# Kernel optimization log

Hardware: AMD Instinct MI355X
Metric: run time of the kernel (lower is better)

## Reference

```python
import jax, jax.numpy as jnp
import numpy as np
from jax import lax

# module hyperparams (from init_kwargs)
IN_C, OUT_C, K, STRIDE, PAD, DIL = 256, 512, 3, 1, 1, 1
IN_SIZE = IN_C * K * K            # 2304
SIZE = 1 << int(np.ceil(np.log2(IN_SIZE)))  # 4096, in_size_extended
NSTACK = int(np.ceil(OUT_C / SIZE))          # 1
BATCH, H, W = 16, 32, 32


def fwht(x):
    """Unnormalized fast Walsh-Hadamard transform along last axis (n = power of 2).
    Matches torch.mm(hadamard(n), x.T).T / cyfht. O(n log n) butterfly."""
    n = x.shape[-1]
    orig_shape = x.shape
    x = x.reshape(-1, n)
    h = 1
    while h < n:
        x = x.reshape(-1, n // (2 * h), 2, h)
        a, b = x[:, :, 0, :], x[:, :, 1, :]
        x = jnp.stack([a + b, a - b], axis=2).reshape(-1, n)
        h *= 2
    return x.reshape(orig_shape)


def setup_inputs() -> dict:
    key = jax.random.key(0)
    k1, k2, k3, k4, k5, k6 = jax.random.split(key, 6)
    inp = jax.random.normal(k1, (BATCH, IN_C, H, W), dtype=jnp.float32)
    # B, G, S ~ N(0, 0.1) as in __init__
    B = 0.1 * jax.random.normal(k2, (NSTACK, SIZE), dtype=jnp.float32)
    G = 0.1 * jax.random.normal(k3, (NSTACK, SIZE), dtype=jnp.float32)
    S = 0.1 * jax.random.normal(k4, (NSTACK, SIZE), dtype=jnp.float32)
    bound = 1.0 / np.sqrt(IN_SIZE)
    bias = jax.random.uniform(k5, (OUT_C,), minval=-bound, maxval=bound, dtype=jnp.float32)
    P = jax.random.permutation(k6, NSTACK * SIZE)  # int32 permutation buffer
    return {"input": inp, "B": B, "G": G, "S": S, "bias": bias, "P": P}


def _pre_process(x):
    b, c, h, w = x.shape
    h_out = (h + 2 * PAD - DIL * (K - 1) - 1) // STRIDE + 1
    w_out = (h + 2 * PAD - DIL * (K - 1) - 1) // STRIDE + 1  # original uses h for w_out too
    # patches: (b, c*K*K, h_out, w_out), feature dim ordered (c, kh, kw) like F.unfold
    patches = lax.conv_general_dilated_patches(
        x, (K, K), (STRIDE, STRIDE), [(PAD, PAD), (PAD, PAD)],
        rhs_dilation=(DIL, DIL), dimension_numbers=("NCHW", "OIHW", "NCHW"))
    # view(b, c, K*K, L).permute(0,3,2,1).reshape(b*L, K*K*c)  -> kk-major, c-minor features
    L = h_out * w_out
    out = patches.reshape(b, c, K * K, L).transpose(0, 3, 2, 1).reshape(b * L, K * K * c)
    out = jnp.pad(out, ((0, 0), (0, SIZE - IN_SIZE)))
    return out, h_out, w_out


def reference(input, B, G, S, bias, P):
    b = input.shape[0]
    x, h_out, w_out = _pre_process(input)          # (b*L, SIZE)
    # diag B (nstack=1), FWHT, permutation, diag G, FWHT, diag S
    x = B.reshape(-1)[None, :] * x
    x = fwht(x)
    x = x[:, P]
    x = G.reshape(-1)[None, :] * x
    x = fwht(x)
    x = S.reshape(-1)[None, :] * x
    out = x[:, :OUT_C] + bias                      # (b*L, OUT_C)
    return out.reshape(b, h_out * w_out, OUT_C).transpose(0, 2, 1).reshape(b, OUT_C, h_out, w_out)
```

## Files before the change

### kernel.cpp

```cpp
#include <hip/hip_runtime.h>
#include <hip/hip_bf16.h>
#include <stdint.h>


typedef _Float16 h2 __attribute__((ext_vector_type(2)));

__device__ __forceinline__ uint16_t f2h16(float f) {
    union { _Float16 h; uint16_t u; } c; c.h = (_Float16)f; return c.u;
}
__device__ __forceinline__ int swz(int j) {
    return j ^ ((j >> 5) & 7) ^ (((j >> 8) & 1) * 24) ^ (((j >> 9) & 1) * 8);
}
__device__ __forceinline__ uint32_t h2u(h2 v) {
    union { h2 h; uint32_t u; } c; c.h = v; return c.u;
}
__device__ __forceinline__ h2 u2h(uint32_t x) {
    union { h2 h; uint32_t u; } c; c.u = x; return c.h;
}
__device__ __forceinline__ h2 pkh(float a, float b) {
    h2 r; r.x = (_Float16)a; r.y = (_Float16)b; return r;
}
__device__ __forceinline__ void h16h(h2* x) {
    #pragma unroll
    for (int h = 1; h < 16; h <<= 1) {
        #pragma unroll
        for (int g = 0; g < 16; g += 2 * h) {
            #pragma unroll
            for (int u = g; u < g + h; ++u) {
                h2 a = x[u], b = x[u + h];
                x[u]     = a + b;
                x[u + h] = a - b;
            }
        }
    }
}
__device__ __forceinline__ void trunc16(const h2* x, h2& s, h2& d) {
    h2 sp[8], sm[8];
    #pragma unroll
    for (int i = 0; i < 8; ++i) {
        sp[i] = x[2 * i] + x[2 * i + 1];
        sm[i] = x[2 * i] - x[2 * i + 1];
    }
    #pragma unroll
    for (int h = 4; h >= 1; h >>= 1) {
        #pragma unroll
        for (int i = 0; i < h; ++i) { sp[i] = sp[i] + sp[i + h]; sm[i] = sm[i] + sm[i + h]; }
    }
    s = sp[0]; d = sm[0];
}

__global__ __launch_bounds__(256, 2)
void fastfood_kernel(const float* __restrict__ in,
                     const float* __restrict__ Bm,
                     const float* __restrict__ Gm,
                     const float* __restrict__ Sm,
                     const float* __restrict__ bias,
                     const int* __restrict__ P,
                     float* __restrict__ out)
{
    __shared__ uint16_t s_in[3 * 8 * 256 * 4];
    __shared__ uint2    buf2[4096];

    const int t  = threadIdx.x;
    const int t1 = t >> 4, t0 = t & 15;
    const int b  = blockIdx.x >> 5;
    const int oh = blockIdx.x & 31;

    #pragma unroll
    for (int i = 0; i < 24; ++i) {
        const int idx   = t + i * 256;
        const int part  = idx & 7;
        const int ch    = (idx >> 3) & 255;
        const int ihrel = idx >> 11;
        const int ih    = oh - 1 + ihrel;
        float4 ld = make_float4(0.f, 0.f, 0.f, 0.f);
        if ((unsigned)ih < 32u) {
            ld = *reinterpret_cast<const float4*>(
                in + ((((size_t)b * 256 + ch) * 32 + ih) * 32 + part * 4));
        }
        const int q    = part >> 1;
        const int slot = (q == 0) ? 0 : (q == 1) ? 2 : (q == 2) ? 1 : 3;
        const int g0   = 4 * (part & 1);
        const int base = (ihrel * 8 + g0) * 1024 + ch * 4 + slot;
        s_in[base       ] = f2h16(ld.x);
        s_in[base + 1024] = f2h16(ld.y);
        s_in[base + 2048] = f2h16(ld.z);
        s_in[base + 3072] = f2h16(ld.w);
    }

    float Bf[9];
    #pragma unroll
    for (int r = 0; r < 9; ++r) Bf[r] = Bm[r * 256 + t];
    h2 Bh[9];
    #pragma unroll
    for (int r = 0; r < 9; ++r) Bh[r] = pkh(Bf[r], Bf[r]);

    h2 Gh[16]; int PAv[16];
    #pragma unroll
    for (int q = 0; q < 4; ++q) {
        const int4   pv = *reinterpret_cast<const int4*>(P + 16 * t + 4 * q);
        const float4 gv = *reinterpret_cast<const float4*>(Gm + 16 * t + 4 * q);
        PAv[4 * q + 0] = swz(pv.x); PAv[4 * q + 1] = swz(pv.y);
        PAv[4 * q + 2] = swz(pv.z); PAv[4 * q + 3] = swz(pv.w);
        Gh[4 * q + 0] = pkh(gv.x, gv.x); Gh[4 * q + 1] = pkh(gv.y, gv.y);
        Gh[4 * q + 2] = pkh(gv.z, gv.z); Gh[4 * q + 3] = pkh(gv.w, gv.w);
    }
    const float St = Sm[t],       Ct = bias[t];
    const float Sd = Sm[256 + t], Cd = bias[256 + t];
    const size_t r0 = ((size_t)b * 512 + t) * 1024 + (size_t)oh * 32;
    const size_t r1 = r0 + (size_t)256 * 1024;
    __syncthreads();

    const uint2* s2 = reinterpret_cast<const uint2*>(s_in);

    for (int p = 0; p < 8; ++p) {
        h2 x0[16], x1[16];
        #pragma unroll
        for (int r = 0; r < 9; ++r) {
            const int kh = r / 3, kw = r % 3;
            const int iw = p - 1 + kw;
            const int g  = iw & 7;
            const uint2 u = s2[(kh * 8 + g) * 256 + t];
            h2 a = u2h(u.x), c = u2h(u.y);
            h2 ta = a, tc = c;
            if (iw < 0) {
                ta.x = (_Float16)0.f; ta.y = c.x;
                tc = a;
            } else if (iw > 7) {
                ta = c;
                tc.x = a.y; tc.y = (_Float16)0.f;
            }
            x0[r] = Bh[r] * ta;
            x1[r] = Bh[r] * tc;
        }
        #pragma unroll
        for (int r = 9; r < 16; ++r) {
            x0[r] = pkh(0.f, 0.f);
            x1[r] = pkh(0.f, 0.f);
        }

        h16h(x0); h16h(x1);
        #pragma unroll
        for (int r = 0; r < 16; ++r)
            buf2[swz(256 * r + t)] = make_uint2(h2u(x0[r]), h2u(x1[r]));
        __syncthreads();
        #pragma unroll
        for (int r = 0; r < 16; ++r) {
            const uint2 u = buf2[swz(256 * t1 + 16 * r + t0)];
            x0[r] = u2h(u.x); x1[r] = u2h(u.y);
        }
        h16h(x0); h16h(x1);
        #pragma unroll
        for (int r = 0; r < 16; ++r)
            buf2[swz(256 * t1 + 16 * r + t0)] = make_uint2(h2u(x0[r]), h2u(x1[r]));
        #pragma unroll
        for (int r = 0; r < 16; ++r) {
            const uint2 u = buf2[swz(256 * t1 + 16 * t0 + r)];
            x0[r] = u2h(u.x); x1[r] = u2h(u.y);
        }
        h16h(x0); h16h(x1);
        #pragma unroll
        for (int r = 0; r < 16; ++r)
            buf2[swz(256 * t1 + 16 * t0 + r)] = make_uint2(h2u(x0[r]), h2u(x1[r]));
        __syncthreads();

        #pragma unroll
        for (int r = 0; r < 16; ++r) {
            const uint2 u = buf2[PAv[r]];
            x0[r] = Gh[r] * u2h(u.x);
            x1[r] = Gh[r] * u2h(u.y);
        }

        h16h(x0); h16h(x1);
        __syncthreads();
        #pragma unroll
        for (int r = 0; r < 16; ++r)
            buf2[swz(256 * t1 + 16 * t0 + r)] = make_uint2(h2u(x0[r]), h2u(x1[r]));
        #pragma unroll
        for (int r = 0; r < 16; ++r) {
            const uint2 u = buf2[swz(256 * t1 + 16 * r + t0)];
            x0[r] = u2h(u.x); x1[r] = u2h(u.y);
        }
        h16h(x0); h16h(x1);
        #pragma unroll
        for (int r = 0; r < 16; ++r)
            buf2[swz(256 * t1 + 16 * r + t0)] = make_uint2(h2u(x0[r]), h2u(x1[r]));
        __syncthreads();
        #pragma unroll
        for (int r = 0; r < 16; ++r) {
            const uint2 u = buf2[swz(256 * r + t)];
            x0[r] = u2h(u.x); x1[r] = u2h(u.y);
        }
        h2 s0, d0, s1, d1;
        trunc16(x0, s0, d0);
        trunc16(x1, s1, d1);

        out[r0 + p]      = St * (float)s0.x + Ct;
        out[r0 + p +  8] = St * (float)s1.x + Ct;
        out[r0 + p + 16] = St * (float)s0.y + Ct;
        out[r0 + p + 24] = St * (float)s1.y + Ct;
        out[r1 + p]      = Sd * (float)d0.x + Cd;
        out[r1 + p +  8] = Sd * (float)d1.x + Cd;
        out[r1 + p + 16] = Sd * (float)d0.y + Cd;
        out[r1 + p + 24] = Sd * (float)d1.y + Cd;
    }
}

extern "C" void kernel_launch(void* const* d_in, const int* in_sizes, int n_in,
                              void* d_out, int out_size, void* d_ws, size_t ws_size,
                              hipStream_t stream) {
    const float* in   = (const float*)d_in[0];
    const float* Bm   = (const float*)d_in[1];
    const float* Gm   = (const float*)d_in[2];
    const float* Sm   = (const float*)d_in[3];
    const float* bias = (const float*)d_in[4];
    const int*   P    = (const int*)d_in[5];
    float* out = (float*)d_out;
    (void)d_ws; (void)ws_size;

    dim3 grid(16 * 32), block(256);
    fastfood_kernel<<<grid, block, 0, stream>>>(in, Bm, Gm, Sm, bias, P, out);
}
```

Before: 148.7 us.

## Stage outputs in LDS and write coalesced float4 rows per output channel

```diff
diff --git a/kernel.cpp b/kernel.cpp
--- a/kernel.cpp
+++ b/kernel.cpp
@@ -47,6 +47,10 @@
         for (int i = 0; i < h; ++i) { sp[i] = sp[i] + sp[i + h]; sm[i] = sm[i] + sm[i + h]; }
     }
     s = sp[0]; d = sm[0];
+}
+__device__ __forceinline__ _Float16 slotk(const uint2& u, int k) {
+    const h2 a = u2h(u.x), c = u2h(u.y);
+    return (k == 0) ? a.x : (k == 1) ? c.x : (k == 2) ? a.y : c.y;
 }
 
 __global__ __launch_bounds__(256, 2)
@@ -105,14 +109,13 @@
         Gh[4 * q + 0] = pkh(gv.x, gv.x); Gh[4 * q + 1] = pkh(gv.y, gv.y);
         Gh[4 * q + 2] = pkh(gv.z, gv.z); Gh[4 * q + 3] = pkh(gv.w, gv.w);
     }
-    const float St = Sm[t],       Ct = bias[t];
-    const float Sd = Sm[256 + t], Cd = bias[256 + t];
-    const size_t r0 = ((size_t)b * 512 + t) * 1024 + (size_t)oh * 32;
-    const size_t r1 = r0 + (size_t)256 * 1024;
     __syncthreads();
 
     const uint2* s2 = reinterpret_cast<const uint2*>(s_in);
 
+    uint2 os[8], od[8];
+
+    #pragma unroll
     for (int p = 0; p < 8; ++p) {
         h2 x0[16], x1[16];
         #pragma unroll
@@ -194,15 +197,44 @@
         h2 s0, d0, s1, d1;
         trunc16(x0, s0, d0);
         trunc16(x1, s1, d1);
-
-        out[r0 + p]      = St * (float)s0.x + Ct;
-        out[r0 + p +  8] = St * (float)s1.x + Ct;
-        out[r0 + p + 16] = St * (float)s0.y + Ct;
-        out[r0 + p + 24] = St * (float)s1.y + Ct;
-        out[r1 + p]      = Sd * (float)d0.x + Cd;
-        out[r1 + p +  8] = Sd * (float)d1.x + Cd;
-        out[r1 + p + 16] = Sd * (float)d0.y + Cd;
-        out[r1 + p + 24] = Sd * (float)d1.y + Cd;
+        os[p] = make_uint2(h2u(s0), h2u(s1));
+        od[p] = make_uint2(h2u(d0), h2u(d1));
+    }
+
+    uint2 U[8], V[8];
+    #pragma unroll
+    for (int i = 0; i < 8; ++i) {
+        const int k = i >> 1, p0 = (i & 1) * 4;
+        h2 lo, hi;
+        lo.x = slotk(os[p0], k);     lo.y = slotk(os[p0 + 1], k);
+        hi.x = slotk(os[p0 + 2], k); hi.y = slotk(os[p0 + 3], k);
+        U[i] = make_uint2(h2u(lo), h2u(hi));
+        lo.x = slotk(od[p0], k);     lo.y = slotk(od[p0 + 1], k);
+        hi.x = slotk(od[p0 + 2], k); hi.y = slotk(od[p0 + 3], k);
+        V[i] = make_uint2(h2u(lo), h2u(hi));
+    }
+
+    __syncthreads();
+    {
+        const int sw = (t >> 1) & 7;
+        #pragma unroll
+        for (int i = 0; i < 8; ++i) {
+            buf2[(size_t)t * 8 + (i ^ sw)]         = U[i];
+            buf2[(size_t)(256 + t) * 8 + (i ^ sw)] = V[i];
+        }
+    }
+    __syncthreads();
+    #pragma unroll
+    for (int it = 0; it < 16; ++it) {
+        const int oc = it * 32 + (t >> 3);
+        const int c  = t & 7;
+        const uint2 u = buf2[(size_t)oc * 8 + (c ^ ((oc >> 1) & 7))];
+        const h2 lo = u2h(u.x), hi = u2h(u.y);
+        const float S = Sm[oc], C = bias[oc];
+        const float4 v = make_float4(S * (float)lo.x + C, S * (float)lo.y + C,
+                                     S * (float)hi.x + C, S * (float)hi.y + C);
+        *reinterpret_cast<float4*>(
+            out + ((size_t)b * 512 + oc) * 1024 + (size_t)oh * 32 + 4 * c) = v;
     }
 }
 
```

Measured after the change: 125.8 us. -15.4%, faster.

## Compute Hadamard butterflies with MFMA 16x16 matrix multiplies and stage output stores

Applied to the files above, without the earlier changes.

```diff
diff --git a/kernel.cpp b/kernel.cpp
--- a/kernel.cpp
+++ b/kernel.cpp
@@ -1,52 +1,41 @@
 #include <hip/hip_runtime.h>
-#include <hip/hip_bf16.h>
 #include <stdint.h>
 
 
-typedef _Float16 h2 __attribute__((ext_vector_type(2)));
+typedef _Float16 h4 __attribute__((ext_vector_type(4)));
+typedef float f4 __attribute__((ext_vector_type(4)));
 
 __device__ __forceinline__ uint16_t f2h16(float f) {
     union { _Float16 h; uint16_t u; } c; c.h = (_Float16)f; return c.u;
 }
-__device__ __forceinline__ int swz(int j) {
-    return j ^ ((j >> 5) & 7) ^ (((j >> 8) & 1) * 24) ^ (((j >> 9) & 1) * 8);
-}
-__device__ __forceinline__ uint32_t h2u(h2 v) {
-    union { h2 h; uint32_t u; } c; c.h = v; return c.u;
-}
-__device__ __forceinline__ h2 u2h(uint32_t x) {
-    union { h2 h; uint32_t u; } c; c.u = x; return c.h;
-}
-__device__ __forceinline__ h2 pkh(float a, float b) {
-    h2 r; r.x = (_Float16)a; r.y = (_Float16)b; return r;
-}
-__device__ __forceinline__ void h16h(h2* x) {
-    #pragma unroll
-    for (int h = 1; h < 16; h <<= 1) {
-        #pragma unroll
-        for (int g = 0; g < 16; g += 2 * h) {
-            #pragma unroll
-            for (int u = g; u < g + h; ++u) {
-                h2 a = x[u], b = x[u + h];
-                x[u]     = a + b;
-                x[u + h] = a - b;
-            }
-        }
-    }
-}
-__device__ __forceinline__ void trunc16(const h2* x, h2& s, h2& d) {
-    h2 sp[8], sm[8];
-    #pragma unroll
-    for (int i = 0; i < 8; ++i) {
-        sp[i] = x[2 * i] + x[2 * i + 1];
-        sm[i] = x[2 * i] - x[2 * i + 1];
-    }
-    #pragma unroll
-    for (int h = 4; h >= 1; h >>= 1) {
-        #pragma unroll
-        for (int i = 0; i < h; ++i) { sp[i] = sp[i] + sp[i + h]; sm[i] = sm[i] + sm[i + h]; }
-    }
-    s = sp[0]; d = sm[0];
+__device__ __forceinline__ float h16f(uint16_t u) {
+    union { _Float16 h; uint16_t u; } c; c.u = u; return (float)c.h;
+}
+__device__ __forceinline__ uint32_t pkh2(float a, float b) {
+    return (uint32_t)f2h16(a) | ((uint32_t)f2h16(b) << 16);
+}
+__device__ __forceinline__ uint32_t lolo(uint32_t a, uint32_t b) {
+    return (a & 0xffffu) | (b << 16);
+}
+__device__ __forceinline__ uint32_t hihi(uint32_t a, uint32_t b) {
+    return (a >> 16) | (b & 0xffff0000u);
+}
+__device__ __forceinline__ h4 u2h4(uint32_t lo, uint32_t hi) {
+    union { h4 h; uint2 u; } c; c.u = make_uint2(lo, hi); return c.h;
+}
+__device__ __forceinline__ uint2 h4u(h4 v) {
+    union { h4 h; uint2 u; } c; c.h = v; return c.u;
+}
+__device__ __forceinline__ h4 cvt4(f4 v) {
+    h4 r; r[0] = (_Float16)v[0]; r[1] = (_Float16)v[1];
+    r[2] = (_Float16)v[2]; r[3] = (_Float16)v[3]; return r;
+}
+__device__ __forceinline__ f4 mfma16(h4 a, h4 b, f4 c) {
+    return __builtin_amdgcn_mfma_f32_16x16x16f16(a, b, c, 0, 0, 0);
+}
+__device__ __forceinline__ int sigma_slot(int j) {
+    const int L = (((j >> 6) & 3) << 4) | (j & 15);
+    return ((j >> 8) << 8) + ((L ^ ((L >> 2) & 3)) << 2) + ((j >> 4) & 3);
 }
 
 __global__ __launch_bounds__(256, 2)
@@ -58,11 +47,12 @@
                      const int* __restrict__ P,
                      float* __restrict__ out)
 {
-    __shared__ uint16_t s_in[3 * 8 * 256 * 4];
-    __shared__ uint2    buf2[4096];
+    __shared__ __align__(16) uint16_t s_in[3 * 8 * 256 * 4];
+    __shared__ __align__(16) uint2    buf2[4096];
 
     const int t  = threadIdx.x;
-    const int t1 = t >> 4, t0 = t & 15;
+    const int l  = t & 63, w = t >> 6;
+    const int c0 = l & 15, ql = l >> 4;
     const int b  = blockIdx.x >> 5;
     const int oh = blockIdx.x & 31;
 
@@ -78,131 +68,201 @@
             ld = *reinterpret_cast<const float4*>(
                 in + ((((size_t)b * 256 + ch) * 32 + ih) * 32 + part * 4));
         }
-        const int q    = part >> 1;
-        const int slot = (q == 0) ? 0 : (q == 1) ? 2 : (q == 2) ? 1 : 3;
-        const int g0   = 4 * (part & 1);
-        const int base = (ihrel * 8 + g0) * 1024 + ch * 4 + slot;
+        const int qq    = part >> 1;
+        const int slotp = (qq == 0) ? 0 : (qq == 1) ? 2 : (qq == 2) ? 1 : 3;
+        const int g0    = 4 * (part & 1);
+        const int chs   = ch ^ (((ch >> 4) & 3) << 2);
+        const int base  = (ihrel * 8 + g0) * 1024 + chs * 4 + slotp;
         s_in[base       ] = f2h16(ld.x);
         s_in[base + 1024] = f2h16(ld.y);
         s_in[base + 2048] = f2h16(ld.z);
         s_in[base + 3072] = f2h16(ld.w);
     }
 
-    float Bf[9];
-    #pragma unroll
-    for (int r = 0; r < 9; ++r) Bf[r] = Bm[r * 256 + t];
-    h2 Bh[9];
-    #pragma unroll
-    for (int r = 0; r < 9; ++r) Bh[r] = pkh(Bf[r], Bf[r]);
-
-    h2 Gh[16]; int PAv[16];
-    #pragma unroll
-    for (int q = 0; q < 4; ++q) {
-        const int4   pv = *reinterpret_cast<const int4*>(P + 16 * t + 4 * q);
-        const float4 gv = *reinterpret_cast<const float4*>(Gm + 16 * t + 4 * q);
-        PAv[4 * q + 0] = swz(pv.x); PAv[4 * q + 1] = swz(pv.y);
-        PAv[4 * q + 2] = swz(pv.z); PAv[4 * q + 3] = swz(pv.w);
-        Gh[4 * q + 0] = pkh(gv.x, gv.x); Gh[4 * q + 1] = pkh(gv.y, gv.y);
-        Gh[4 * q + 2] = pkh(gv.z, gv.z); Gh[4 * q + 3] = pkh(gv.w, gv.w);
-    }
-    const float St = Sm[t],       Ct = bias[t];
-    const float Sd = Sm[256 + t], Cd = bias[256 + t];
-    const size_t r0 = ((size_t)b * 512 + t) * 1024 + (size_t)oh * 32;
-    const size_t r1 = r0 + (size_t)256 * 1024;
+    h4 Hp, Hn;
+    #pragma unroll
+    for (int i = 0; i < 4; ++i) {
+        const int k = 4 * ql + i;
+        const float s = (__popc(c0 & k) & 1) ? -1.f : 1.f;
+        Hp[i] = (_Float16)s; Hn[i] = (_Float16)(-s);
+    }
+    h4 Bh[9];
+    #pragma unroll
+    for (int kk = 0; kk < 9; ++kk) {
+        const float4 v = *reinterpret_cast<const float4*>(Bm + 256 * kk + 16 * c0 + 4 * ql);
+        Bh[kk][0] = (_Float16)v.x; Bh[kk][1] = (_Float16)v.y;
+        Bh[kk][2] = (_Float16)v.z; Bh[kk][3] = (_Float16)v.w;
+    }
+    h4 Gh[16];
+    #pragma unroll
+    for (int a = 0; a < 16; ++a) {
+        const float4 v = *reinterpret_cast<const float4*>(Gm + 256 * a + 16 * c0 + 4 * ql);
+        Gh[a][0] = (_Float16)v.x; Gh[a][1] = (_Float16)v.y;
+        Gh[a][2] = (_Float16)v.z; Gh[a][3] = (_Float16)v.w;
+    }
     __syncthreads();
 
     const uint2* s2 = reinterpret_cast<const uint2*>(s_in);
-
-    for (int p = 0; p < 8; ++p) {
-        h2 x0[16], x1[16];
-        #pragma unroll
-        for (int r = 0; r < 9; ++r) {
-            const int kh = r / 3, kw = r % 3;
+    const int Lsw = l ^ ((l >> 2) & 3);
+    const f4 zf = {0.f, 0.f, 0.f, 0.f};
+    uint2 os[2][4], od[2][4];
+
+    #pragma unroll
+    for (int rq = 0; rq < 2; ++rq) {
+        const int p = w + 4 * rq;
+
+        h4 st[16][4];
+        #pragma unroll
+        for (int kk = 0; kk < 9; ++kk) {
+            const int kh = kk / 3, kw = kk % 3;
             const int iw = p - 1 + kw;
             const int g  = iw & 7;
-            const uint2 u = s2[(kh * 8 + g) * 256 + t];
-            h2 a = u2h(u.x), c = u2h(u.y);
-            h2 ta = a, tc = c;
-            if (iw < 0) {
-                ta.x = (_Float16)0.f; ta.y = c.x;
-                tc = a;
-            } else if (iw > 7) {
-                ta = c;
-                tc.x = a.y; tc.y = (_Float16)0.f;
-            }
-            x0[r] = Bh[r] * ta;
-            x1[r] = Bh[r] * tc;
-        }
-        #pragma unroll
-        for (int r = 9; r < 16; ++r) {
-            x0[r] = pkh(0.f, 0.f);
-            x1[r] = pkh(0.f, 0.f);
-        }
-
-        h16h(x0); h16h(x1);
-        #pragma unroll
-        for (int r = 0; r < 16; ++r)
-            buf2[swz(256 * r + t)] = make_uint2(h2u(x0[r]), h2u(x1[r]));
-        __syncthreads();
-        #pragma unroll
-        for (int r = 0; r < 16; ++r) {
-            const uint2 u = buf2[swz(256 * t1 + 16 * r + t0)];
-            x0[r] = u2h(u.x); x1[r] = u2h(u.y);
-        }
-        h16h(x0); h16h(x1);
-        #pragma unroll
-        for (int r = 0; r < 16; ++r)
-            buf2[swz(256 * t1 + 16 * r + t0)] = make_uint2(h2u(x0[r]), h2u(x1[r]));
-        #pragma unroll
-        for (int r = 0; r < 16; ++r) {
-            const uint2 u = buf2[swz(256 * t1 + 16 * t0 + r)];
-            x0[r] = u2h(u.x); x1[r] = u2h(u.y);
-        }
-        h16h(x0); h16h(x1);
-        #pragma unroll
-        for (int r = 0; r < 16; ++r)
-            buf2[swz(256 * t1 + 16 * t0 + r)] = make_uint2(h2u(x0[r]), h2u(x1[r]));
-        __syncthreads();
-
-        #pragma unroll
-        for (int r = 0; r < 16; ++r) {
-            const uint2 u = buf2[PAv[r]];
-            x0[r] = Gh[r] * u2h(u.x);
-            x1[r] = Gh[r] * u2h(u.y);
-        }
-
-        h16h(x0); h16h(x1);
-        __syncthreads();
-        #pragma unroll
-        for (int r = 0; r < 16; ++r)
-            buf2[swz(256 * t1 + 16 * t0 + r)] = make_uint2(h2u(x0[r]), h2u(x1[r]));
-        #pragma unroll
-        for (int r = 0; r < 16; ++r) {
-            const uint2 u = buf2[swz(256 * t1 + 16 * r + t0)];
-            x0[r] = u2h(u.x); x1[r] = u2h(u.y);
-        }
-        h16h(x0); h16h(x1);
-        #pragma unroll
-        for (int r = 0; r < 16; ++r)
-            buf2[swz(256 * t1 + 16 * r + t0)] = make_uint2(h2u(x0[r]), h2u(x1[r]));
-        __syncthreads();
-        #pragma unroll
-        for (int r = 0; r < 16; ++r) {
-            const uint2 u = buf2[swz(256 * r + t)];
-            x0[r] = u2h(u.x); x1[r] = u2h(u.y);
-        }
-        h2 s0, d0, s1, d1;
-        trunc16(x0, s0, d0);
-        trunc16(x1, s1, d1);
-
-        out[r0 + p]      = St * (float)s0.x + Ct;
-        out[r0 + p +  8] = St * (float)s1.x + Ct;
-        out[r0 + p + 16] = St * (float)s0.y + Ct;
-        out[r0 + p + 24] = St * (float)s1.y + Ct;
-        out[r1 + p]      = Sd * (float)d0.x + Cd;
-        out[r1 + p +  8] = Sd * (float)d1.x + Cd;
-        out[r1 + p + 16] = Sd * (float)d0.y + Cd;
-        out[r1 + p + 24] = Sd * (float)d1.y + Cd;
+            const int sb = (kh * 8 + g) * 256 + 16 * c0 + 4 * (ql ^ (c0 & 3));
+            const uint4 r01 = *reinterpret_cast<const uint4*>(s2 + sb);
+            const uint4 r23 = *reinterpret_cast<const uint4*>(s2 + sb + 2);
+            uint32_t x0 = r01.x, y0 = r01.y, x1 = r01.z, y1 = r01.w;
+            uint32_t x2 = r23.x, y2 = r23.y, x3 = r23.z, y3 = r23.w;
+            if (kw == 0 && iw < 0) {
+                uint32_t tp;
+                tp = x0; x0 = y0 << 16; y0 = tp;
+                tp = x1; x1 = y1 << 16; y1 = tp;
+                tp = x2; x2 = y2 << 16; y2 = tp;
+                tp = x3; x3 = y3 << 16; y3 = tp;
+            } else if (kw == 2 && iw > 7) {
+                uint32_t tp;
+                tp = x0; x0 = y0; y0 = tp >> 16;
+                tp = x1; x1 = y1; y1 = tp >> 16;
+                tp = x2; x2 = y2; y2 = tp >> 16;
+                tp = x3; x3 = y3; y3 = tp >> 16;
+            }
+            h4 fr[4];
+            fr[0] = u2h4(lolo(x0, x1), lolo(x2, x3)) * Bh[kk];
+            fr[1] = u2h4(lolo(y0, y1), lolo(y2, y3)) * Bh[kk];
+            fr[2] = u2h4(hihi(x0, x1), hihi(x2, x3)) * Bh[kk];
+            fr[3] = u2h4(hihi(y0, y1), hihi(y2, y3)) * Bh[kk];
+            #pragma unroll
+            for (int px = 0; px < 4; ++px) {
+                const f4 d1 = mfma16(fr[px], Hp, zf);
+                const h4 h1 = cvt4(d1);
+                const f4 d2 = mfma16(Hp, h1, zf);
+                st[kk][px] = cvt4(d2);
+            }
+        }
+        {
+            const h4 z4 = {(_Float16)0.f, (_Float16)0.f, (_Float16)0.f, (_Float16)0.f};
+            #pragma unroll
+            for (int kk = 9; kk < 16; ++kk) {
+                st[kk][0] = z4; st[kk][1] = z4; st[kk][2] = z4; st[kk][3] = z4;
+            }
+        }
+
+        #pragma unroll
+        for (int hh = 1; hh < 16; hh <<= 1) {
+            #pragma unroll
+            for (int gg = 0; gg < 16; gg += 2 * hh) {
+                #pragma unroll
+                for (int u = gg; u < gg + hh; ++u) {
+                    #pragma unroll
+                    for (int px = 0; px < 4; ++px) {
+                        const h4 A = st[u][px], Bv = st[u + hh][px];
+                        st[u][px]      = A + Bv;
+                        st[u + hh][px] = A - Bv;
+                    }
+                }
+            }
+        }
+
+        uint2 garr[16][4];
+        #pragma unroll
+        for (int s = 0; s < 4; ++s) {
+            if (w == s) {
+                int4 Pv[16];
+                #pragma unroll
+                for (int a = 0; a < 8; ++a)
+                    Pv[a] = *reinterpret_cast<const int4*>(P + 256 * a + 16 * c0 + 4 * ql);
+                #pragma unroll
+                for (int a = 0; a < 16; ++a) {
+                    const uint2 UA = h4u(st[a][0]), UB = h4u(st[a][1]);
+                    const uint2 UC = h4u(st[a][2]), UD = h4u(st[a][3]);
+                    uint4* dst = reinterpret_cast<uint4*>(&buf2[256 * a + 4 * Lsw]);
+                    dst[0] = make_uint4(lolo(UA.x, UC.x), lolo(UB.x, UD.x),
+                                        hihi(UA.x, UC.x), hihi(UB.x, UD.x));
+                    dst[1] = make_uint4(lolo(UA.y, UC.y), lolo(UB.y, UD.y),
+                                        hihi(UA.y, UC.y), hihi(UB.y, UD.y));
+                }
+                #pragma unroll
+                for (int a = 8; a < 16; ++a)
+                    Pv[a] = *reinterpret_cast<const int4*>(P + 256 * a + 16 * c0 + 4 * ql);
+                #pragma unroll
+                for (int a = 0; a < 16; ++a) {
+                    const int pj0 = Pv[a].x, pj1 = Pv[a].y, pj2 = Pv[a].z, pj3 = Pv[a].w;
+                    garr[a][0] = buf2[sigma_slot(pj0)];
+                    garr[a][1] = buf2[sigma_slot(pj1)];
+                    garr[a][2] = buf2[sigma_slot(pj2)];
+                    garr[a][3] = buf2[sigma_slot(pj3)];
+                }
+            }
+            __syncthreads();
+        }
+
+        f4 sa[4] = {zf, zf, zf, zf}, da[4] = {zf, zf, zf, zf};
+        #pragma unroll
+        for (int a = 0; a < 16; ++a) {
+            const uint32_t gx0 = garr[a][0].x, gy0 = garr[a][0].y;
+            const uint32_t gx1 = garr[a][1].x, gy1 = garr[a][1].y;
+            const uint32_t gx2 = garr[a][2].x, gy2 = garr[a][2].y;
+            const uint32_t gx3 = garr[a][3].x, gy3 = garr[a][3].y;
+            h4 fr[4];
+            fr[0] = u2h4(lolo(gx0, gx1), lolo(gx2, gx3)) * Gh[a];
+            fr[1] = u2h4(lolo(gy0, gy1), lolo(gy2, gy3)) * Gh[a];
+            fr[2] = u2h4(hihi(gx0, gx1), hihi(gx2, gx3)) * Gh[a];
+            fr[3] = u2h4(hihi(gy0, gy1), hihi(gy2, gy3)) * Gh[a];
+            const h4 HA = (a & 1) ? Hn : Hp;
+            #pragma unroll
+            for (int px = 0; px < 4; ++px) {
+                const f4 d1 = mfma16(fr[px], Hp, zf);
+                const h4 h1 = cvt4(d1);
+                sa[px] = mfma16(Hp, h1, sa[px]);
+                da[px] = mfma16(HA, h1, da[px]);
+            }
+        }
+        #pragma unroll
+        for (int i = 0; i < 4; ++i) {
+            os[rq][i] = make_uint2(pkh2(sa[0][i], sa[2][i]), pkh2(sa[1][i], sa[3][i]));
+            od[rq][i] = make_uint2(pkh2(da[0][i], da[2][i]), pkh2(da[1][i], da[3][i]));
+        }
+    }
+
+    __syncthreads();
+    #pragma unroll
+    for (int rq = 0; rq < 2; ++rq) {
+        const int g = w + 4 * rq;
+        #pragma unroll
+        for (int i = 0; i < 4; ++i) {
+            const int oc0 = 64 * ql + 16 * i + c0;
+            buf2[oc0 * 8 + (g ^ ((oc0 >> 1) & 7))] = os[rq][i];
+            const int oc1 = oc0 + 256;
+            buf2[oc1 * 8 + (g ^ ((oc1 >> 1) & 7))] = od[rq][i];
+        }
+    }
+    __syncthreads();
+    #pragma unroll
+    for (int it = 0; it < 16; ++it) {
+        const int oc = it * 32 + (t >> 3), c = t & 7;
+        const float S = Sm[oc], C = bias[oc];
+        float o[4];
+        #pragma unroll
+        for (int e = 0; e < 4; ++e) {
+            const int ow = 4 * c + e, gg = ow & 7, sh = ow >> 3;
+            const uint2 u = buf2[oc * 8 + (gg ^ ((oc >> 1) & 7))];
+            const uint32_t word = (sh & 1) ? u.y : u.x;
+            const uint16_t hb = (sh >> 1) ? (uint16_t)(word >> 16)
+                                          : (uint16_t)(word & 0xffffu);
+            o[e] = S * h16f(hb) + C;
+        }
+        *reinterpret_cast<float4*>(
+            out + ((size_t)b * 512 + oc) * 1024 + (size_t)oh * 32 + 4 * c)
+            = make_float4(o[0], o[1], o[2], o[3]);
     }
 }
 
```

New measurement: 184.9 us. +24.3%, slower.
